# Kernel optimization log

Hardware: AMD Instinct MI355X
Metric: run time of the kernel (lower is better)

## Reference

```python
import jax, jax.numpy as jnp
import numpy as np

L, D, H, DH, S, B, V = 8, 1024, 16, 64, 1024, 4, 32000
EPS = 1e-5


def layernorm(x, s, b):
    m = x.mean(-1, keepdims=True)
    v = ((x - m) ** 2).mean(-1, keepdims=True)
    return (x - m) * jax.lax.rsqrt(v + EPS) * s + b


def setup_inputs() -> dict:
    key = jax.random.key(0)
    ks = jax.random.split(key, 12)
    sd = 0.02
    inp = {
        'idx': jax.random.randint(ks[0], (B, S), 0, V),
        'tok_emb': jax.random.normal(ks[1], (V, D), jnp.float32) * sd,
        'pos_emb': jax.random.normal(ks[2], (S, D), jnp.float32) * sd,
        'ln1_s': jnp.ones((L, D), jnp.float32),
        'ln1_b': jnp.zeros((L, D), jnp.float32),
        'wq': jax.random.normal(ks[3], (L, H, D, DH), jnp.float32) * sd,
        'wk': jax.random.normal(ks[4], (L, H, D, DH), jnp.float32) * sd,
        'wv': jax.random.normal(ks[5], (L, H, D, DH), jnp.float32) * sd,
        'wproj': jax.random.normal(ks[6], (L, D, D), jnp.float32) * sd,  # stored [D_in, D_out]
        'ln2_s': jnp.ones((L, D), jnp.float32),
        'ln2_b': jnp.zeros((L, D), jnp.float32),
        'w1': jax.random.normal(ks[7], (L, D, 4 * D), jnp.float32) * sd,
        'b1': jnp.zeros((L, 4 * D), jnp.float32),
        'w2': jax.random.normal(ks[8], (L, 4 * D, D), jnp.float32) * sd,
        'b2': jnp.zeros((L, D), jnp.float32),
        'lnf_s': jnp.ones((D,), jnp.float32),
        'lnf_b': jnp.zeros((D,), jnp.float32),
        'lm_w': jax.random.normal(ks[9], (D, V), jnp.float32) * sd,  # stored [D_in, V]
        'lm_b': jnp.zeros((V,), jnp.float32),
    }
    return inp


def reference(idx, tok_emb, pos_emb, ln1_s, ln1_b, wq, wk, wv, wproj,
              ln2_s, ln2_b, w1, b1, w2, b2, lnf_s, lnf_b, lm_w, lm_b):
    T = idx.shape[1]
    x = tok_emb[idx] + pos_emb[:T]  # [B,T,D]
    mask = jnp.tril(jnp.ones((T, T), bool))
    scale = DH ** -0.5
    for l in range(L):  # fixed small layer count
        h = layernorm(x, ln1_s[l], ln1_b[l])
        q = jnp.einsum('bsd,hde->bhse', h, wq[l])
        k = jnp.einsum('bsd,hde->bhse', h, wk[l])
        v = jnp.einsum('bsd,hde->bhse', h, wv[l])
        att = jnp.einsum('bhse,bhte->bhst', q, k) * scale
        att = jnp.where(mask, att, -jnp.inf)
        att = jax.nn.softmax(att, axis=-1)  # dropout=0.0 -> identity
        o = jnp.einsum('bhst,bhte->bhse', att, v)
        o = o.transpose(0, 2, 1, 3).reshape(x.shape)  # concat heads: [B,T,H*DH]
        x = x + o @ wproj[l]
        h2 = layernorm(x, ln2_s[l], ln2_b[l])
        x = x + jax.nn.relu(h2 @ w1[l] + b1[l]) @ w2[l] + b2[l]
    x = layernorm(x, lnf_s, lnf_b)
    logits = x @ lm_w + lm_b  # [B,T,V]
    return logits
```

## Files before the change

kernel.cpp:

```cpp
#include <hip/hip_runtime.h>
#include <hip/hip_bf16.h>

#define LL 8
#define DD 1024
#define HH 16
#define DHH 64
#define SS 1024
#define BB 4
#define VV 32000
#define MM (BB * SS)

typedef unsigned short u16;
typedef __attribute__((ext_vector_type(8))) short short8v;
typedef __attribute__((ext_vector_type(4))) float f32x4;
typedef unsigned int __attribute__((address_space(1))) guint;
typedef unsigned int __attribute__((address_space(3))) luint;

__device__ __forceinline__ float bf2f_lo(unsigned u) { return __uint_as_float(u << 16); }
__device__ __forceinline__ u16 f2bf(float f) {
  unsigned x = __float_as_uint(f);
  return (u16)((x + 0x7fffu + ((x >> 16) & 1u)) >> 16);
}

__global__ __launch_bounds__(256) void embed_kernel(
    const int* __restrict__ idx, const float* __restrict__ tok,
    const float* __restrict__ pos, float* __restrict__ x) {
  int i = blockIdx.x * blockDim.x + threadIdx.x;
  int elem = i * 4;
  int row = elem / DD;
  int d = elem % DD;
  int s = row % SS;
  int t = idx[row];
  float4 tv = *(const float4*)(tok + (size_t)t * DD + d);
  float4 pv = *(const float4*)(pos + (size_t)s * DD + d);
  tv.x += pv.x; tv.y += pv.y; tv.z += pv.z; tv.w += pv.w;
  *(float4*)(x + (size_t)elem) = tv;
}

__global__ __launch_bounds__(256) void ln_bf16_kernel(
    const float* __restrict__ x, const float* __restrict__ sc,
    const float* __restrict__ bi, u16* __restrict__ out) {
  const int row = blockIdx.x;
  const int tid = threadIdx.x;
  __shared__ float red[4];
  float4 v = ((const float4*)(x + (size_t)row * DD))[tid];
  float s = v.x + v.y + v.z + v.w;
  #pragma unroll
  for (int off = 32; off; off >>= 1) s += __shfl_down(s, off);
  if ((tid & 63) == 0) red[tid >> 6] = s;
  __syncthreads();
  float mean = (red[0] + red[1] + red[2] + red[3]) * (1.f / DD);
  float dx = v.x - mean, dy = v.y - mean, dz = v.z - mean, dw = v.w - mean;
  float vs = dx * dx + dy * dy + dz * dz + dw * dw;
  __syncthreads();
  #pragma unroll
  for (int off = 32; off; off >>= 1) vs += __shfl_down(vs, off);
  if ((tid & 63) == 0) red[tid >> 6] = vs;
  __syncthreads();
  float var = (red[0] + red[1] + red[2] + red[3]) * (1.f / DD);
  float rstd = rsqrtf(var + 1e-5f);
  float4 s4 = ((const float4*)sc)[tid];
  float4 b4 = ((const float4*)bi)[tid];
  ushort4 o;
  o.x = f2bf(dx * rstd * s4.x + b4.x);
  o.y = f2bf(dy * rstd * s4.y + b4.y);
  o.z = f2bf(dz * rstd * s4.z + b4.z);
  o.w = f2bf(dw * rstd * s4.w + b4.w);
  *(ushort4*)(out + (size_t)row * DD + tid * 4) = o;
}

template <bool HEADW>
__global__ __launch_bounds__(256) void convT_kernel(
    const float* __restrict__ W, u16* __restrict__ BT, int K, int N,
    size_t lstride) {
  __shared__ float tile[32][33];
  const int n0 = blockIdx.x * 32, k0 = blockIdx.y * 32, l = blockIdx.z;
  const int tx = threadIdx.x & 31, ty = threadIdx.x >> 5;
  const float* Wl;
  int ld;
  if (HEADW) {
    const int h = n0 >> 6;
    Wl = W + ((size_t)(l * HH + h) * K) * 64 + (n0 & 63);
    ld = 64;
  } else {
    Wl = W + (size_t)l * K * N + n0;
    ld = N;
  }
  #pragma unroll
  for (int i = 0; i < 4; ++i)
    tile[ty + 8 * i][tx] = Wl[(size_t)(k0 + ty + 8 * i) * ld + tx];
  __syncthreads();
  u16* out = BT + (size_t)l * lstride;
  #pragma unroll
  for (int i = 0; i < 4; ++i)
    out[(size_t)(n0 + ty + 8 * i) * K + k0 + tx] = f2bf(tile[tx][ty + 8 * i]);
}

__global__ __launch_bounds__(256) void transpose_v(
    const u16* __restrict__ qkv, u16* __restrict__ vt) {
  __shared__ u16 t[32][33];
  const int s0 = blockIdx.x * 32, d0 = blockIdx.y * 32;
  const int tx = threadIdx.x & 31, ty = threadIdx.x >> 5;
  #pragma unroll
  for (int i = 0; i < 4; ++i)
    t[ty + 8 * i][tx] = qkv[(size_t)(s0 + ty + 8 * i) * 3072 + 2048 + d0 + tx];
  __syncthreads();
  #pragma unroll
  for (int i = 0; i < 4; ++i)
    vt[(size_t)(d0 + ty + 8 * i) * MM + s0 + tx] = t[tx][ty + 8 * i];
}

template <bool BIAS, bool RELU, bool RESID, bool OBF16>
__global__ __launch_bounds__(256) void gemm_mfma(
    const u16* __restrict__ A, const u16* __restrict__ BT,
    const float* __restrict__ bias, const float* __restrict__ resid,
    void* __restrict__ Cv, int M, int N, int K) {
  __shared__ u16 As[128 * 64];
  __shared__ u16 Bs[128 * 64];
  const int tid = threadIdx.x;
  const int lane = tid & 63, wave = tid >> 6;
  const int m0 = blockIdx.x * 128, n0 = blockIdx.y * 128;
  const int wr = (wave >> 1) * 64, wc = (wave & 1) * 64;
  const int srow = tid >> 3;
  const int scol = (((tid & 7) ^ (srow & 7)) * 8);
  const u16* Ag = A + (size_t)(m0 + srow) * K + scol;
  const u16* Bg = BT + (size_t)(n0 + srow) * K + scol;

  f32x4 acc[4][4] = {};
  for (int k0 = 0; k0 < K; k0 += 64) {
    #pragma unroll
    for (int c = 0; c < 4; ++c) {
      __builtin_amdgcn_global_load_lds(
          (const guint*)(Ag + k0 + (size_t)c * 32 * K),
          (luint*)(As + c * 2048 + tid * 8), 16, 0, 0);
      __builtin_amdgcn_global_load_lds(
          (const guint*)(Bg + k0 + (size_t)c * 32 * K),
          (luint*)(Bs + c * 2048 + tid * 8), 16, 0, 0);
    }
    __syncthreads();
    #pragma unroll
    for (int kk = 0; kk < 64; kk += 32) {
      const int chA = (((kk >> 3) | (lane >> 4)) ^ (lane & 7)) * 8;
      short8v av[4], bv[4];
      #pragma unroll
      for (int i = 0; i < 4; ++i)
        av[i] = *(const short8v*)(As + (wr + i * 16 + (lane & 15)) * 64 + chA);
      #pragma unroll
      for (int j = 0; j < 4; ++j)
        bv[j] = *(const short8v*)(Bs + (wc + j * 16 + (lane & 15)) * 64 + chA);
      #pragma unroll
      for (int i = 0; i < 4; ++i)
        #pragma unroll
        for (int j = 0; j < 4; ++j)
          acc[i][j] = __builtin_amdgcn_mfma_f32_16x16x32_bf16(av[i], bv[j], acc[i][j], 0, 0, 0);
    }
    __syncthreads();
  }
  #pragma unroll
  for (int i = 0; i < 4; ++i) {
    #pragma unroll
    for (int j = 0; j < 4; ++j) {
      const int col = n0 + wc + j * 16 + (lane & 15);
      #pragma unroll
      for (int r = 0; r < 4; ++r) {
        const int row = m0 + wr + i * 16 + (lane >> 4) * 4 + r;
        float v = acc[i][j][r];
        if (BIAS) v += bias[col];
        if (RELU) v = fmaxf(v, 0.f);
        if (RESID) v += resid[(size_t)row * N + col];
        if (OBF16)
          ((u16*)Cv)[(size_t)row * N + col] = f2bf(v);
        else
          ((float*)Cv)[(size_t)row * N + col] = v;
      }
    }
  }
}

#define LDA_(BUF, KH, F) \
  (*(const short8v*)&As[BUF][KH][(wm * 128 + (F) * 16 + (lane & 15)) * 32 + rg])
#define LDB_(BUF, KH, NF) \
  (*(const short8v*)&Bs[BUF][KH][(wn * 64 + (NF) * 16 + (lane & 15)) * 32 + rg])
#define LDS_A(S0,S1,S2,S3, BUF, KH, FB) { \
  S0 = LDA_(BUF, KH, (FB) + 0); S1 = LDA_(BUF, KH, (FB) + 1); \
  S2 = LDA_(BUF, KH, (FB) + 2); S3 = LDA_(BUF, KH, (FB) + 3); }
#define LDS_B(S0,S1,S2,S3, BUF, KH) { \
  S0 = LDB_(BUF, KH, 0); S1 = LDB_(BUF, KH, 1); \
  S2 = LDB_(BUF, KH, 2); S3 = LDB_(BUF, KH, 3); }
#define STAGE_A(BUF, KH, KT) do { \
  __builtin_amdgcn_global_load_lds((const guint*)(Abase + (KT) * 64 + (KH) * 32), \
      (luint*)(&As[BUF][KH][tid * 8]), 16, 0, 0); \
  __builtin_amdgcn_global_load_lds((const guint*)(Abase + (size_t)128 * K + (KT) * 64 + (KH) * 32), \
      (luint*)(&As[BUF][KH][(tid + 512) * 8]), 16, 0, 0); \
} while (0)
#define STAGE_B(BUF, KH, KT) do { \
  __builtin_amdgcn_global_load_lds((const guint*)(Bbase + (KT) * 64 + (KH) * 32), \
      (luint*)(&Bs[BUF][KH][tid * 8]), 16, 0, 0); \
  __builtin_amdgcn_global_load_lds((const guint*)(Bbase + (size_t)128 * K + (KT) * 64 + (KH) * 32), \
      (luint*)(&Bs[BUF][KH][(tid + 512) * 8]), 16, 0, 0); \
} while (0)
#define MROW(F, AQ, B0,B1,B2,B3) \
  acc[F][0] = __builtin_amdgcn_mfma_f32_16x16x32_bf16(AQ, B0, acc[F][0], 0, 0, 0); \
  acc[F][1] = __builtin_amdgcn_mfma_f32_16x16x32_bf16(AQ, B1, acc[F][1], 0, 0, 0); \
  acc[F][2] = __builtin_amdgcn_mfma_f32_16x16x32_bf16(AQ, B2, acc[F][2], 0, 0, 0); \
  acc[F][3] = __builtin_amdgcn_mfma_f32_16x16x32_bf16(AQ, B3, acc[F][3], 0, 0, 0);
#define MFMA16S(FB, A0,A1,A2,A3, B0,B1,B2,B3) \
  MROW((FB) + 0, A0, B0,B1,B2,B3) MROW((FB) + 1, A1, B0,B1,B2,B3) \
  MROW((FB) + 2, A2, B0,B1,B2,B3) MROW((FB) + 3, A3, B0,B1,B2,B3)
#define BARRIER __builtin_amdgcn_s_barrier()
#define MEMFENCE asm volatile("" ::: "memory")

#define TILE4(CUR, KT, ST1, ST2, V1STR, V3STR, LD4, LGK4STR) { \
  const int cur_ = (CUR); \
  MEMFENCE; \
  LDS_A(aN0,aN1,aN2,aN3, cur_, 0, 4); \
  if (ST1) { STAGE_A(cur_ ^ 1, 1, (KT) + 1); } \
  asm volatile("s_waitcnt " V1STR ::: "memory"); \
  asm volatile("s_waitcnt lgkmcnt(4)" ::: "memory"); \
  BARRIER; \
  __builtin_amdgcn_s_setprio(1); \
  MFMA16S(0, aP0,aP1,aP2,aP3, bP0,bP1,bP2,bP3); \
  __builtin_amdgcn_s_setprio(0); \
  MEMFENCE; \
  LDS_A(aP0,aP1,aP2,aP3, cur_, 1, 0); \
  LDS_B(bN0,bN1,bN2,bN3, cur_, 1); \
  if (ST1) { STAGE_B(cur_ ^ 1, 1, (KT) + 1); } \
  asm volatile("s_waitcnt lgkmcnt(8)" ::: "memory"); \
  BARRIER; \
  __builtin_amdgcn_s_setprio(1); \
  MFMA16S(4, aN0,aN1,aN2,aN3, bP0,bP1,bP2,bP3); \
  __builtin_amdgcn_s_setprio(0); \
  MEMFENCE; \
  LDS_A(aN0,aN1,aN2,aN3, cur_, 1, 4); \
  if (ST2) { STAGE_A(cur_, 0, (KT) + 2); } \
  asm volatile("s_waitcnt " V3STR ::: "memory"); \
  asm volatile("s_waitcnt lgkmcnt(4)" ::: "memory"); \
  BARRIER; \
  __builtin_amdgcn_s_setprio(1); \
  MFMA16S(0, aP0,aP1,aP2,aP3, bN0,bN1,bN2,bN3); \
  __builtin_amdgcn_s_setprio(0); \
  MEMFENCE; \
  if (LD4) { LDS_A(aP0,aP1,aP2,aP3, cur_ ^ 1, 0, 0); \
             LDS_B(bP0,bP1,bP2,bP3, cur_ ^ 1, 0); } \
  if (ST2) { STAGE_B(cur_, 0, (KT) + 2); } \
  asm volatile("s_waitcnt " LGK4STR ::: "memory"); \
  BARRIER; \
  __builtin_amdgcn_s_setprio(1); \
  MFMA16S(4, aN0,aN1,aN2,aN3, bN0,bN1,bN2,bN3); \
  __builtin_amdgcn_s_setprio(0); \
}

template <bool BIAS, bool RELU, bool RESID, bool OBF16, bool NTC>
__global__ __launch_bounds__(512, 2) void gemm8(
    const u16* __restrict__ A, const u16* __restrict__ BT,
    const float* __restrict__ bias, const float* __restrict__ resid,
    void* __restrict__ Cv, int M, int N, int K) {
  __shared__ u16 As[2][2][8192];
  __shared__ u16 Bs[2][2][8192];
  const int tid = threadIdx.x;
  const int lane = tid & 63, wave = tid >> 6;
  const int wm = wave >> 2, wn = wave & 3;
  const int nwg = gridDim.x;
  const int bid = blockIdx.x;
  const int wg = ((nwg & 7) == 0) ? ((bid & 7) * (nwg >> 3) + (bid >> 3)) : bid;
  const int nmt = M >> 8;
  const int m0 = (wg % nmt) * 256;
  const int n0 = (wg / nmt) * 256;
  const int NT = K >> 6;
  const int sr = tid >> 2;
  const int ssc = (((tid & 3) ^ ((tid >> 3) & 3)) * 8);
  const u16* Abase = A + (size_t)(m0 + sr) * K + ssc;
  const u16* Bbase = BT + (size_t)(n0 + sr) * K + ssc;
  const int rg = (((lane >> 4) ^ ((lane >> 1) & 3)) * 8);

  f32x4 acc[8][4] = {};
  short8v aP0, aP1, aP2, aP3, aN0, aN1, aN2, aN3;
  short8v bP0, bP1, bP2, bP3, bN0, bN1, bN2, bN3;

  STAGE_A(0, 0, 0); STAGE_B(0, 0, 0);
  STAGE_A(0, 1, 0); STAGE_B(0, 1, 0);
  STAGE_A(1, 0, 1); STAGE_B(1, 0, 1);
  asm volatile("s_waitcnt vmcnt(8)" ::: "memory");
  BARRIER;
  MEMFENCE;
  LDS_A(aP0,aP1,aP2,aP3, 0, 0, 0);
  LDS_B(bP0,bP1,bP2,bP3, 0, 0);

  int kt = 0;
  for (; kt < NT - 2; ++kt) {
    TILE4(kt & 1, kt, true, true, "vmcnt(6)", "vmcnt(6)", true, "lgkmcnt(8)");
  }
  TILE4(kt & 1, kt, true, false, "vmcnt(6)", "vmcnt(4)", true, "lgkmcnt(8)");
  ++kt;
  TILE4(kt & 1, kt, false, false, "vmcnt(0)", "vmcnt(0)", false, "lgkmcnt(0)");

  #pragma unroll
  for (int f = 0; f < 8; ++f) {
    #pragma unroll
    for (int n = 0; n < 4; ++n) {
      const int col = n0 + wn * 64 + n * 16 + (lane & 15);
      #pragma unroll
      for (int r = 0; r < 4; ++r) {
        const int row = m0 + wm * 128 + f * 16 + (lane >> 4) * 4 + r;
        float v = acc[f][n][r];
        if (BIAS) v += bias[col];
        if (RELU) v = fmaxf(v, 0.f);
        if (RESID) v += resid[(size_t)row * N + col];
        if (OBF16) {
          u16 val = f2bf(v);
          if (NTC) __builtin_nontemporal_store(val, &((u16*)Cv)[(size_t)row * N + col]);
          else ((u16*)Cv)[(size_t)row * N + col] = val;
        } else {
          if (NTC) __builtin_nontemporal_store(v, &((float*)Cv)[(size_t)row * N + col]);
          else ((float*)Cv)[(size_t)row * N + col] = v;
        }
      }
    }
  }
}

__global__ __launch_bounds__(256) void gemm_fb(
    const u16* __restrict__ A, const float* __restrict__ B,
    const float* __restrict__ bias, float* __restrict__ C, int M, int N, int K) {
  __shared__ alignas(16) float Asm[16][68];
  __shared__ alignas(16) float Bsm[16][68];
  const int tid = threadIdx.x;
  const int tx = tid & 15, ty = tid >> 4;
  const int m0 = blockIdx.y * 64, n0 = blockIdx.x * 64;
  const int ar = tid >> 2, ac = (tid & 3) * 4;
  const int br = tid >> 4, bc = (tid & 15) * 4;
  float acc[4][4] = {};
  for (int k0 = 0; k0 < K; k0 += 16) {
    ushort4 au = *(const ushort4*)(A + (size_t)(m0 + ar) * K + k0 + ac);
    float4 bv = *(const float4*)(B + (size_t)(k0 + br) * N + n0 + bc);
    Asm[ac + 0][ar] = bf2f_lo(au.x);
    Asm[ac + 1][ar] = bf2f_lo(au.y);
    Asm[ac + 2][ar] = bf2f_lo(au.z);
    Asm[ac + 3][ar] = bf2f_lo(au.w);
    *(float4*)&Bsm[br][bc] = bv;
    __syncthreads();
    #pragma unroll
    for (int kk = 0; kk < 16; ++kk) {
      float4 a = *(const float4*)&Asm[kk][ty * 4];
      float4 b = *(const float4*)&Bsm[kk][tx * 4];
      acc[0][0] += a.x * b.x; acc[0][1] += a.x * b.y; acc[0][2] += a.x * b.z; acc[0][3] += a.x * b.w;
      acc[1][0] += a.y * b.x; acc[1][1] += a.y * b.y; acc[1][2] += a.y * b.z; acc[1][3] += a.y * b.w;
      acc[2][0] += a.z * b.x; acc[2][1] += a.z * b.y; acc[2][2] += a.z * b.z; acc[2][3] += a.z * b.w;
      acc[3][0] += a.w * b.x; acc[3][1] += a.w * b.y; acc[3][2] += a.w * b.z; acc[3][3] += a.w * b.w;
    }
    __syncthreads();
  }
  #pragma unroll
  for (int i = 0; i < 4; ++i) {
    const int m = m0 + ty * 4 + i;
    #pragma unroll
    for (int j = 0; j < 4; ++j) {
      const int n = n0 + tx * 4 + j;
      __builtin_nontemporal_store(acc[i][j] + bias[n], &C[(size_t)m * N + n]);
    }
  }
}

__global__ __launch_bounds__(256) void attn_mfma(
    const u16* __restrict__ qkv, const u16* __restrict__ vt,
    u16* __restrict__ o) {
  __shared__ alignas(16) u16 Ksh[64 * 64];
  __shared__ alignas(16) u16 Vsh[64 * 64];
  __shared__ unsigned Plds[4][16 * 41];
  __shared__ float bcast[4][16];
  const int tid = threadIdx.x;
  const int lane = tid & 63, wave = tid >> 6;
  const int g = lane >> 4, qi = lane & 15;
  const int qt = blockIdx.x, h = blockIdx.y, b = blockIdx.z;
  const int q0w = qt * 64 + wave * 16;
  const int qloc = wave * 16 + qi;

  short8v qf0, qf1;
  {
    const u16* qp = qkv + ((size_t)b * SS + q0w + qi) * 3072 + h * DHH + g * 8;
    qf0 = *(const short8v*)qp;
    qf1 = *(const short8v*)(qp + 32);
  }

  f32x4 oacc[4] = {};
  float mrow = -1e30f, lrow = 0.f;

  for (int kt = 0; kt <= qt; ++kt) {
    __syncthreads();
    #pragma unroll
    for (int u = 0; u < 2; ++u) {
      const int unit = tid + 256 * u;
      const int row = unit >> 3, ch = unit & 7;
      const int sch = ch ^ (row & 7);
      __builtin_amdgcn_global_load_lds(
          (const guint*)(qkv + ((size_t)b * SS + kt * 64 + row) * 3072 + 1024 + h * DHH + sch * 8),
          (luint*)(Ksh + unit * 8), 16, 0, 0);
      __builtin_amdgcn_global_load_lds(
          (const guint*)(vt + ((size_t)(h * DHH + row)) * MM + b * SS + kt * 64 + sch * 8),
          (luint*)(Vsh + unit * 8), 16, 0, 0);
    }
    __syncthreads();

    f32x4 st[4] = {};
    #pragma unroll
    for (int t = 0; t < 4; ++t) {
      const int row = t * 16 + qi;
      const int swz = (row & 7) << 4;
      short8v kf0 = *(const short8v*)(Ksh + row * 64 + (((g * 16) ^ swz) >> 1));
      short8v kf1 = *(const short8v*)(Ksh + row * 64 + (((64 + g * 16) ^ swz) >> 1));
      st[t] = __builtin_amdgcn_mfma_f32_16x16x32_bf16(kf0, qf0, st[t], 0, 0, 0);
      st[t] = __builtin_amdgcn_mfma_f32_16x16x32_bf16(kf1, qf1, st[t], 0, 0, 0);
    }

    if (kt == qt) {
      #pragma unroll
      for (int t = 0; t < 4; ++t)
        #pragma unroll
        for (int r = 0; r < 4; ++r)
          if (t * 16 + 4 * g + r > qloc) st[t][r] = -1e30f;
    }

    float mt = st[0][0];
    #pragma unroll
    for (int t = 0; t < 4; ++t)
      #pragma unroll
      for (int r = 0; r < 4; ++r) mt = fmaxf(mt, st[t][r]);
    mt = fmaxf(mt, __shfl_xor(mt, 16));
    mt = fmaxf(mt, __shfl_xor(mt, 32));
    const float mnew = fmaxf(mrow, mt * 0.125f);
    const float corr = __expf(mrow - mnew);
    float pl = 0.f;
    #pragma unroll
    for (int t = 0; t < 4; ++t) {
      #pragma unroll
      for (int r2 = 0; r2 < 2; ++r2) {
        float plo = __expf(fmaf(st[t][2 * r2], 0.125f, -mnew));
        float phi = __expf(fmaf(st[t][2 * r2 + 1], 0.125f, -mnew));
        pl += plo + phi;
        Plds[wave][qi * 41 + 8 * t + 2 * g + r2] =
            (unsigned)f2bf(plo) | ((unsigned)f2bf(phi) << 16);
      }
    }
    pl += __shfl_xor(pl, 16);
    pl += __shfl_xor(pl, 32);
    lrow = lrow * corr + pl;
    mrow = mnew;

    if (g == 0) bcast[wave][qi] = corr;
    float c0 = bcast[wave][g * 4 + 0];
    float c1 = bcast[wave][g * 4 + 1];
    float c2 = bcast[wave][g * 4 + 2];
    float c3 = bcast[wave][g * 4 + 3];
    #pragma unroll
    for (int dvt = 0; dvt < 4; ++dvt) {
      oacc[dvt][0] *= c0; oacc[dvt][1] *= c1;
      oacc[dvt][2] *= c2; oacc[dvt][3] *= c3;
    }

    union U8 { unsigned u[4]; short8v s8; };
    U8 pa0, pa1;
    #pragma unroll
    for (int c = 0; c < 4; ++c) {
      pa0.u[c] = Plds[wave][qi * 41 + g * 4 + c];
      pa1.u[c] = Plds[wave][qi * 41 + 16 + g * 4 + c];
    }
    #pragma unroll
    for (int dvt = 0; dvt < 4; ++dvt) {
      const int row = dvt * 16 + qi;
      const int swz = (row & 7) << 4;
      short8v v0 = *(const short8v*)(Vsh + row * 64 + (((g * 16) ^ swz) >> 1));
      short8v v1 = *(const short8v*)(Vsh + row * 64 + (((64 + g * 16) ^ swz) >> 1));
      oacc[dvt] = __builtin_amdgcn_mfma_f32_16x16x32_bf16(pa0.s8, v0, oacc[dvt], 0, 0, 0);
      oacc[dvt] = __builtin_amdgcn_mfma_f32_16x16x32_bf16(pa1.s8, v1, oacc[dvt], 0, 0, 0);
    }
  }

  if (g == 0) bcast[wave][qi] = 1.f / lrow;
  float i0 = bcast[wave][g * 4 + 0];
  float i1 = bcast[wave][g * 4 + 1];
  float i2 = bcast[wave][g * 4 + 2];
  float i3 = bcast[wave][g * 4 + 3];
  #pragma unroll
  for (int dvt = 0; dvt < 4; ++dvt) {
    const int col = h * DHH + dvt * 16 + qi;
    o[((size_t)b * SS + q0w + g * 4 + 0) * DD + col] = f2bf(oacc[dvt][0] * i0);
    o[((size_t)b * SS + q0w + g * 4 + 1) * DD + col] = f2bf(oacc[dvt][1] * i1);
    o[((size_t)b * SS + q0w + g * 4 + 2) * DD + col] = f2bf(oacc[dvt][2] * i2);
    o[((size_t)b * SS + q0w + g * 4 + 3) * DD + col] = f2bf(oacc[dvt][3] * i3);
  }
}

extern "C" void kernel_launch(void* const* d_in, const int* in_sizes, int n_in,
                              void* d_out, int out_size, void* d_ws, size_t ws_size,
                              hipStream_t stream) {
  const int* idx = (const int*)d_in[0];
  const float* tok_emb = (const float*)d_in[1];
  const float* pos_emb = (const float*)d_in[2];
  const float* ln1_s = (const float*)d_in[3];
  const float* ln1_b = (const float*)d_in[4];
  const float* wq = (const float*)d_in[5];
  const float* wk = (const float*)d_in[6];
  const float* wv = (const float*)d_in[7];
  const float* wproj = (const float*)d_in[8];
  const float* ln2_s = (const float*)d_in[9];
  const float* ln2_b = (const float*)d_in[10];
  const float* w1 = (const float*)d_in[11];
  const float* b1 = (const float*)d_in[12];
  const float* w2 = (const float*)d_in[13];
  const float* b2 = (const float*)d_in[14];
  const float* lnf_s = (const float*)d_in[15];
  const float* lnf_b = (const float*)d_in[16];
  const float* lm_w = (const float*)d_in[17];
  const float* lm_b = (const float*)d_in[18];

  const size_t MD = (size_t)MM * DD;

  u16* sc0 = (u16*)d_out;
  u16* BTqkv = sc0;
  u16* BTp = BTqkv + (size_t)LL * 3072 * DD;
  u16* BTw1 = BTp + (size_t)LL * DD * DD;
  u16* BTw2 = BTw1 + (size_t)LL * DD * 4 * DD;
  u16* qkvb = BTw2 + (size_t)LL * DD * 4 * DD;
  u16* vtb = qkvb + (size_t)MM * 3072;
  u16* ob = vtb + MD;
  u16* tmp = ob + MD;

  float* x = (float*)d_ws;
  u16* h = (u16*)((char*)d_ws + MD * 4);
  u16* BTlm = (u16*)((char*)d_ws + MD * 4 + MD * 2);
  const bool big_ws = ws_size >= (MD * 4 + MD * 2 + (size_t)VV * DD * 2);

  const dim3 blk(256);

  convT_kernel<true><<<dim3(DD / 32, DD / 32, LL), blk, 0, stream>>>(
      wq, BTqkv, DD, DD, (size_t)3072 * DD);
  convT_kernel<true><<<dim3(DD / 32, DD / 32, LL), blk, 0, stream>>>(
      wk, BTqkv + (size_t)DD * DD, DD, DD, (size_t)3072 * DD);
  convT_kernel<true><<<dim3(DD / 32, DD / 32, LL), blk, 0, stream>>>(
      wv, BTqkv + (size_t)2 * DD * DD, DD, DD, (size_t)3072 * DD);
  convT_kernel<false><<<dim3(DD / 32, DD / 32, LL), blk, 0, stream>>>(
      wproj, BTp, DD, DD, (size_t)DD * DD);
  convT_kernel<false><<<dim3(4 * DD / 32, DD / 32, LL), blk, 0, stream>>>(
      w1, BTw1, DD, 4 * DD, (size_t)DD * 4 * DD);
  convT_kernel<false><<<dim3(DD / 32, 4 * DD / 32, LL), blk, 0, stream>>>(
      w2, BTw2, 4 * DD, DD, (size_t)4 * DD * DD);
  if (big_ws)
    convT_kernel<false><<<dim3(VV / 32, DD / 32, 1), blk, 0, stream>>>(
        lm_w, BTlm, DD, VV, (size_t)VV * DD);

  embed_kernel<<<(MM * DD / 4 + 255) / 256, blk, 0, stream>>>(idx, tok_emb, pos_emb, x);

  for (int l = 0; l < LL; ++l) {
    ln_bf16_kernel<<<MM, blk, 0, stream>>>(x, ln1_s + l * DD, ln1_b + l * DD, h);
    gemm8<false, false, false, true, false><<<dim3((MM / 256) * (3072 / 256)), dim3(512), 0, stream>>>(
        h, BTqkv + (size_t)l * 3072 * DD, nullptr, nullptr, qkvb, MM, 3072, DD);
    transpose_v<<<dim3(MM / 32, DD / 32), blk, 0, stream>>>(qkvb, vtb);
    attn_mfma<<<dim3(SS / 64, HH, BB), blk, 0, stream>>>(qkvb, vtb, ob);
    gemm_mfma<false, false, true, false><<<dim3(MM / 128, DD / 128), blk, 0, stream>>>(
        ob, BTp + (size_t)l * DD * DD, nullptr, x, x, MM, DD, DD);
    ln_bf16_kernel<<<MM, blk, 0, stream>>>(x, ln2_s + l * DD, ln2_b + l * DD, h);
    gemm8<true, true, false, true, true><<<dim3((MM / 256) * (4 * DD / 256)), dim3(512), 0, stream>>>(
        h, BTw1 + (size_t)l * DD * 4 * DD, b1 + (size_t)l * 4 * DD, nullptr, tmp,
        MM, 4 * DD, DD);
    gemm_mfma<true, false, true, false><<<dim3(MM / 128, DD / 128), blk, 0, stream>>>(
        tmp, BTw2 + (size_t)l * 4 * DD * DD, b2 + (size_t)l * DD, x, x, MM, DD, 4 * DD);
  }

  ln_bf16_kernel<<<MM, blk, 0, stream>>>(x, lnf_s, lnf_b, h);
  if (big_ws) {
    gemm8<true, false, false, false, true><<<dim3((MM / 256) * (VV / 256)), dim3(512), 0, stream>>>(
        h, BTlm, lm_b, nullptr, (float*)d_out, MM, VV, DD);
  } else {
    gemm_fb<<<dim3(VV / 64, MM / 64), blk, 0, stream>>>(
        h, lm_w, lm_b, (float*)d_out, MM, VV, DD);
  }
}
```

Before: 2.621 ms.

## Replace simple MFMA GEMM with pipelined 128x128 kernel for proj and FFN2

Adds gemm4p, a 256-thread 128x128-tile GEMM using the same double-buffered, split-K-half, barrier-interleaved LDS staging scheme as gemm8. It replaces the single-buffer gemm_mfma for the attention projection and second FFN GEMM, aiming to overlap global loads with MFMA work. The change also drops the nontemporal stores from the gemm8 epilogues and from the fallback GEMM, so outputs now use normal cached stores. The main risk is that the hand-tuned waitcnt values and raised register pressure from launch_bounds(256,2) may hurt occupancy.

New measurement: 2.429 ms. 7.3% less time.

```diff
diff --git a/kernel.cpp b/kernel.cpp
--- a/kernel.cpp
+++ b/kernel.cpp
@@ -110,72 +110,8 @@
     vt[(size_t)(d0 + ty + 8 * i) * MM + s0 + tx] = t[tx][ty + 8 * i];
 }
 
-template <bool BIAS, bool RELU, bool RESID, bool OBF16>
-__global__ __launch_bounds__(256) void gemm_mfma(
-    const u16* __restrict__ A, const u16* __restrict__ BT,
-    const float* __restrict__ bias, const float* __restrict__ resid,
-    void* __restrict__ Cv, int M, int N, int K) {
-  __shared__ u16 As[128 * 64];
-  __shared__ u16 Bs[128 * 64];
-  const int tid = threadIdx.x;
-  const int lane = tid & 63, wave = tid >> 6;
-  const int m0 = blockIdx.x * 128, n0 = blockIdx.y * 128;
-  const int wr = (wave >> 1) * 64, wc = (wave & 1) * 64;
-  const int srow = tid >> 3;
-  const int scol = (((tid & 7) ^ (srow & 7)) * 8);
-  const u16* Ag = A + (size_t)(m0 + srow) * K + scol;
-  const u16* Bg = BT + (size_t)(n0 + srow) * K + scol;
-
-  f32x4 acc[4][4] = {};
-  for (int k0 = 0; k0 < K; k0 += 64) {
-    #pragma unroll
-    for (int c = 0; c < 4; ++c) {
-      __builtin_amdgcn_global_load_lds(
-          (const guint*)(Ag + k0 + (size_t)c * 32 * K),
-          (luint*)(As + c * 2048 + tid * 8), 16, 0, 0);
-      __builtin_amdgcn_global_load_lds(
-          (const guint*)(Bg + k0 + (size_t)c * 32 * K),
-          (luint*)(Bs + c * 2048 + tid * 8), 16, 0, 0);
-    }
-    __syncthreads();
-    #pragma unroll
-    for (int kk = 0; kk < 64; kk += 32) {
-      const int chA = (((kk >> 3) | (lane >> 4)) ^ (lane & 7)) * 8;
-      short8v av[4], bv[4];
-      #pragma unroll
-      for (int i = 0; i < 4; ++i)
-        av[i] = *(const short8v*)(As + (wr + i * 16 + (lane & 15)) * 64 + chA);
-      #pragma unroll
-      for (int j = 0; j < 4; ++j)
-        bv[j] = *(const short8v*)(Bs + (wc + j * 16 + (lane & 15)) * 64 + chA);
-      #pragma unroll
-      for (int i = 0; i < 4; ++i)
-        #pragma unroll
-        for (int j = 0; j < 4; ++j)
-          acc[i][j] = __builtin_amdgcn_mfma_f32_16x16x32_bf16(av[i], bv[j], acc[i][j], 0, 0, 0);
-    }
-    __syncthreads();
-  }
-  #pragma unroll
-  for (int i = 0; i < 4; ++i) {
-    #pragma unroll
-    for (int j = 0; j < 4; ++j) {
-      const int col = n0 + wc + j * 16 + (lane & 15);
-      #pragma unroll
-      for (int r = 0; r < 4; ++r) {
-        const int row = m0 + wr + i * 16 + (lane >> 4) * 4 + r;
-        float v = acc[i][j][r];
-        if (BIAS) v += bias[col];
-        if (RELU) v = fmaxf(v, 0.f);
-        if (RESID) v += resid[(size_t)row * N + col];
-        if (OBF16)
-          ((u16*)Cv)[(size_t)row * N + col] = f2bf(v);
-        else
-          ((float*)Cv)[(size_t)row * N + col] = v;
-      }
-    }
-  }
-}
+#define BARRIER __builtin_amdgcn_s_barrier()
+#define MEMFENCE asm volatile("" ::: "memory")
 
 #define LDA_(BUF, KH, F) \
   (*(const short8v*)&As[BUF][KH][(wm * 128 + (F) * 16 + (lane & 15)) * 32 + rg])
@@ -207,11 +143,10 @@
 #define MFMA16S(FB, A0,A1,A2,A3, B0,B1,B2,B3) \
   MROW((FB) + 0, A0, B0,B1,B2,B3) MROW((FB) + 1, A1, B0,B1,B2,B3) \
   MROW((FB) + 2, A2, B0,B1,B2,B3) MROW((FB) + 3, A3, B0,B1,B2,B3)
-#define BARRIER __builtin_amdgcn_s_barrier()
-#define MEMFENCE asm volatile("" ::: "memory")
 
 #define TILE4(CUR, KT, ST1, ST2, V1STR, V3STR, LD4, LGK4STR) { \
   const int cur_ = (CUR); \
+   \
   MEMFENCE; \
   LDS_A(aN0,aN1,aN2,aN3, cur_, 0, 4); \
   if (ST1) { STAGE_A(cur_ ^ 1, 1, (KT) + 1); } \
@@ -221,6 +156,7 @@
   __builtin_amdgcn_s_setprio(1); \
   MFMA16S(0, aP0,aP1,aP2,aP3, bP0,bP1,bP2,bP3); \
   __builtin_amdgcn_s_setprio(0); \
+   \
   MEMFENCE; \
   LDS_A(aP0,aP1,aP2,aP3, cur_, 1, 0); \
   LDS_B(bN0,bN1,bN2,bN3, cur_, 1); \
@@ -230,6 +166,7 @@
   __builtin_amdgcn_s_setprio(1); \
   MFMA16S(4, aN0,aN1,aN2,aN3, bP0,bP1,bP2,bP3); \
   __builtin_amdgcn_s_setprio(0); \
+   \
   MEMFENCE; \
   LDS_A(aN0,aN1,aN2,aN3, cur_, 1, 4); \
   if (ST2) { STAGE_A(cur_, 0, (KT) + 2); } \
@@ -239,6 +176,7 @@
   __builtin_amdgcn_s_setprio(1); \
   MFMA16S(0, aP0,aP1,aP2,aP3, bN0,bN1,bN2,bN3); \
   __builtin_amdgcn_s_setprio(0); \
+   \
   MEMFENCE; \
   if (LD4) { LDS_A(aP0,aP1,aP2,aP3, cur_ ^ 1, 0, 0); \
              LDS_B(bP0,bP1,bP2,bP3, cur_ ^ 1, 0); } \
@@ -250,7 +188,7 @@
   __builtin_amdgcn_s_setprio(0); \
 }
 
-template <bool BIAS, bool RELU, bool RESID, bool OBF16, bool NTC>
+template <bool BIAS, bool RELU, bool RESID, bool OBF16>
 __global__ __launch_bounds__(512, 2) void gemm8(
     const u16* __restrict__ A, const u16* __restrict__ BT,
     const float* __restrict__ bias, const float* __restrict__ resid,
@@ -306,14 +244,136 @@
         if (BIAS) v += bias[col];
         if (RELU) v = fmaxf(v, 0.f);
         if (RESID) v += resid[(size_t)row * N + col];
-        if (OBF16) {
-          u16 val = f2bf(v);
-          if (NTC) __builtin_nontemporal_store(val, &((u16*)Cv)[(size_t)row * N + col]);
-          else ((u16*)Cv)[(size_t)row * N + col] = val;
-        } else {
-          if (NTC) __builtin_nontemporal_store(v, &((float*)Cv)[(size_t)row * N + col]);
-          else ((float*)Cv)[(size_t)row * N + col] = v;
-        }
+        if (OBF16)
+          ((u16*)Cv)[(size_t)row * N + col] = f2bf(v);
+        else
+          ((float*)Cv)[(size_t)row * N + col] = v;
+      }
+    }
+  }
+}
+
+#define LDA4_(BUF, KH, F) \
+  (*(const short8v*)&As[BUF][KH][(wm * 64 + (F) * 16 + (lane & 15)) * 32 + rg])
+#define LDB4_(BUF, KH, NF) \
+  (*(const short8v*)&Bs[BUF][KH][(wn * 64 + (NF) * 16 + (lane & 15)) * 32 + rg])
+#define STAGE_A4(BUF, KH, KT) do { \
+  __builtin_amdgcn_global_load_lds((const guint*)(Abase + (KT) * 64 + (KH) * 32), \
+      (luint*)(&As[BUF][KH][tid * 8]), 16, 0, 0); \
+  __builtin_amdgcn_global_load_lds((const guint*)(Abase + (size_t)64 * K + (KT) * 64 + (KH) * 32), \
+      (luint*)(&As[BUF][KH][(tid + 256) * 8]), 16, 0, 0); \
+} while (0)
+#define STAGE_B4(BUF, KH, KT) do { \
+  __builtin_amdgcn_global_load_lds((const guint*)(Bbase + (KT) * 64 + (KH) * 32), \
+      (luint*)(&Bs[BUF][KH][tid * 8]), 16, 0, 0); \
+  __builtin_amdgcn_global_load_lds((const guint*)(Bbase + (size_t)64 * K + (KT) * 64 + (KH) * 32), \
+      (luint*)(&Bs[BUF][KH][(tid + 256) * 8]), 16, 0, 0); \
+} while (0)
+#define MFMA8S(F0, F1, A0, A1, B0,B1,B2,B3) \
+  MROW(F0, A0, B0,B1,B2,B3) MROW(F1, A1, B0,B1,B2,B3)
+
+#define TILE4P(CUR, KT, ST1, ST2, V1STR, V3STR, LD4, LGK4STR) { \
+  const int cur_ = (CUR); \
+   \
+  MEMFENCE; \
+  aN0 = LDA4_(cur_, 0, 2); aN1 = LDA4_(cur_, 0, 3); \
+  if (ST1) { STAGE_A4(cur_ ^ 1, 1, (KT) + 1); } \
+  asm volatile("s_waitcnt " V1STR ::: "memory"); \
+  asm volatile("s_waitcnt lgkmcnt(2)" ::: "memory"); \
+  BARRIER; \
+  __builtin_amdgcn_s_setprio(1); \
+  MFMA8S(0, 1, aP0, aP1, bP0,bP1,bP2,bP3); \
+  __builtin_amdgcn_s_setprio(0); \
+   \
+  MEMFENCE; \
+  aP0 = LDA4_(cur_, 1, 0); aP1 = LDA4_(cur_, 1, 1); \
+  bN0 = LDB4_(cur_, 1, 0); bN1 = LDB4_(cur_, 1, 1); \
+  bN2 = LDB4_(cur_, 1, 2); bN3 = LDB4_(cur_, 1, 3); \
+  if (ST1) { STAGE_B4(cur_ ^ 1, 1, (KT) + 1); } \
+  asm volatile("s_waitcnt lgkmcnt(6)" ::: "memory"); \
+  BARRIER; \
+  __builtin_amdgcn_s_setprio(1); \
+  MFMA8S(2, 3, aN0, aN1, bP0,bP1,bP2,bP3); \
+  __builtin_amdgcn_s_setprio(0); \
+   \
+  MEMFENCE; \
+  aN0 = LDA4_(cur_, 1, 2); aN1 = LDA4_(cur_, 1, 3); \
+  if (ST2) { STAGE_A4(cur_, 0, (KT) + 2); } \
+  asm volatile("s_waitcnt " V3STR ::: "memory"); \
+  asm volatile("s_waitcnt lgkmcnt(2)" ::: "memory"); \
+  BARRIER; \
+  __builtin_amdgcn_s_setprio(1); \
+  MFMA8S(0, 1, aP0, aP1, bN0,bN1,bN2,bN3); \
+  __builtin_amdgcn_s_setprio(0); \
+   \
+  MEMFENCE; \
+  if (LD4) { aP0 = LDA4_(cur_ ^ 1, 0, 0); aP1 = LDA4_(cur_ ^ 1, 0, 1); \
+             bP0 = LDB4_(cur_ ^ 1, 0, 0); bP1 = LDB4_(cur_ ^ 1, 0, 1); \
+             bP2 = LDB4_(cur_ ^ 1, 0, 2); bP3 = LDB4_(cur_ ^ 1, 0, 3); } \
+  if (ST2) { STAGE_B4(cur_, 0, (KT) + 2); } \
+  asm volatile("s_waitcnt " LGK4STR ::: "memory"); \
+  BARRIER; \
+  __builtin_amdgcn_s_setprio(1); \
+  MFMA8S(2, 3, aN0, aN1, bN0,bN1,bN2,bN3); \
+  __builtin_amdgcn_s_setprio(0); \
+}
+
+template <bool BIAS, bool RELU, bool RESID, bool OBF16>
+__global__ __launch_bounds__(256, 2) void gemm4p(
+    const u16* __restrict__ A, const u16* __restrict__ BT,
+    const float* __restrict__ bias, const float* __restrict__ resid,
+    void* __restrict__ Cv, int M, int N, int K) {
+  __shared__ u16 As[2][2][4096];
+  __shared__ u16 Bs[2][2][4096];
+  const int tid = threadIdx.x;
+  const int lane = tid & 63, wave = tid >> 6;
+  const int wm = wave >> 1, wn = wave & 1;
+  const int m0 = blockIdx.x * 128, n0 = blockIdx.y * 128;
+  const int NT = K >> 6;
+  const int sr = tid >> 2;
+  const int ssc = (((tid & 3) ^ ((tid >> 3) & 3)) * 8);
+  const u16* Abase = A + (size_t)(m0 + sr) * K + ssc;
+  const u16* Bbase = BT + (size_t)(n0 + sr) * K + ssc;
+  const int rg = (((lane >> 4) ^ ((lane >> 1) & 3)) * 8);
+
+  f32x4 acc[4][4] = {};
+  short8v aP0, aP1, aN0, aN1;
+  short8v bP0, bP1, bP2, bP3, bN0, bN1, bN2, bN3;
+
+  STAGE_A4(0, 0, 0); STAGE_B4(0, 0, 0);
+  STAGE_A4(0, 1, 0); STAGE_B4(0, 1, 0);
+  STAGE_A4(1, 0, 1); STAGE_B4(1, 0, 1);
+  asm volatile("s_waitcnt vmcnt(8)" ::: "memory");
+  BARRIER;
+  MEMFENCE;
+  aP0 = LDA4_(0, 0, 0); aP1 = LDA4_(0, 0, 1);
+  bP0 = LDB4_(0, 0, 0); bP1 = LDB4_(0, 0, 1);
+  bP2 = LDB4_(0, 0, 2); bP3 = LDB4_(0, 0, 3);
+
+  int kt = 0;
+  for (; kt < NT - 2; ++kt) {
+    TILE4P(kt & 1, kt, true, true, "vmcnt(6)", "vmcnt(6)", true, "lgkmcnt(6)");
+  }
+  TILE4P(kt & 1, kt, true, false, "vmcnt(6)", "vmcnt(4)", true, "lgkmcnt(6)");
+  ++kt;
+  TILE4P(kt & 1, kt, false, false, "vmcnt(0)", "vmcnt(0)", false, "lgkmcnt(0)");
+
+  #pragma unroll
+  for (int f = 0; f < 4; ++f) {
+    #pragma unroll
+    for (int n = 0; n < 4; ++n) {
+      const int col = n0 + wn * 64 + n * 16 + (lane & 15);
+      #pragma unroll
+      for (int r = 0; r < 4; ++r) {
+        const int row = m0 + wm * 64 + f * 16 + (lane >> 4) * 4 + r;
+        float v = acc[f][n][r];
+        if (BIAS) v += bias[col];
+        if (RELU) v = fmaxf(v, 0.f);
+        if (RESID) v += resid[(size_t)row * N + col];
+        if (OBF16)
+          ((u16*)Cv)[(size_t)row * N + col] = f2bf(v);
+        else
+          ((float*)Cv)[(size_t)row * N + col] = v;
       }
     }
   }
@@ -356,7 +416,7 @@
     #pragma unroll
     for (int j = 0; j < 4; ++j) {
       const int n = n0 + tx * 4 + j;
-      __builtin_nontemporal_store(acc[i][j] + bias[n], &C[(size_t)m * N + n]);
+      C[(size_t)m * N + n] = acc[i][j] + bias[n];
     }
   }
 }
@@ -552,23 +612,23 @@
 
   for (int l = 0; l < LL; ++l) {
     ln_bf16_kernel<<<MM, blk, 0, stream>>>(x, ln1_s + l * DD, ln1_b + l * DD, h);
-    gemm8<false, false, false, true, false><<<dim3((MM / 256) * (3072 / 256)), dim3(512), 0, stream>>>(
+    gemm8<false, false, false, true><<<dim3((MM / 256) * (3072 / 256)), dim3(512), 0, stream>>>(
         h, BTqkv + (size_t)l * 3072 * DD, nullptr, nullptr, qkvb, MM, 3072, DD);
     transpose_v<<<dim3(MM / 32, DD / 32), blk, 0, stream>>>(qkvb, vtb);
     attn_mfma<<<dim3(SS / 64, HH, BB), blk, 0, stream>>>(qkvb, vtb, ob);
-    gemm_mfma<false, false, true, false><<<dim3(MM / 128, DD / 128), blk, 0, stream>>>(
+    gemm4p<false, false, true, false><<<dim3(MM / 128, DD / 128), blk, 0, stream>>>(
         ob, BTp + (size_t)l * DD * DD, nullptr, x, x, MM, DD, DD);
     ln_bf16_kernel<<<MM, blk, 0, stream>>>(x, ln2_s + l * DD, ln2_b + l * DD, h);
-    gemm8<true, true, false, true, true><<<dim3((MM / 256) * (4 * DD / 256)), dim3(512), 0, stream>>>(
+    gemm8<true, true, false, true><<<dim3((MM / 256) * (4 * DD / 256)), dim3(512), 0, stream>>>(
         h, BTw1 + (size_t)l * DD * 4 * DD, b1 + (size_t)l * 4 * DD, nullptr, tmp,
         MM, 4 * DD, DD);
-    gemm_mfma<true, false, true, false><<<dim3(MM / 128, DD / 128), blk, 0, stream>>>(
+    gemm4p<true, false, true, false><<<dim3(MM / 128, DD / 128), blk, 0, stream>>>(
         tmp, BTw2 + (size_t)l * 4 * DD * DD, b2 + (size_t)l * DD, x, x, MM, DD, 4 * DD);
   }
 
   ln_bf16_kernel<<<MM, blk, 0, stream>>>(x, lnf_s, lnf_b, h);
   if (big_ws) {
-    gemm8<true, false, false, false, true><<<dim3((MM / 256) * (VV / 256)), dim3(512), 0, stream>>>(
+    gemm8<true, false, false, false><<<dim3((MM / 256) * (VV / 256)), dim3(512), 0, stream>>>(
         h, BTlm, lm_b, nullptr, (float*)d_out, MM, VV, DD);
   } else {
     gemm_fb<<<dim3(VV / 64, MM / 64), blk, 0, stream>>>(
```
